# Performance work log

Hardware: AMD Instinct MI355X
Metric: run time of the kernel (lower is better)

Reference implementation:

```python
import jax, jax.numpy as jnp
import numpy as np

HEADS = 4
DIM_HEAD = 32
EPS = 1e-5


def setup_inputs() -> dict:
    key = jax.random.key(0)
    ks = jax.random.split(key, 4)
    B, dim, H, W = 8, 256, 128, 128
    hidden = HEADS * DIM_HEAD  # 128
    x = jax.random.normal(ks[0], (B, dim, H, W), dtype=jnp.float32)
    # 1x1 conv weights stored as [out_ch, in_ch]
    qkv_w = jax.random.normal(ks[1], (3 * hidden, dim), dtype=jnp.float32) * (1.0 / np.sqrt(dim))
    conv_w = jax.random.normal(ks[2], (dim, hidden), dtype=jnp.float32) * (1.0 / np.sqrt(hidden))
    conv_b = jax.random.normal(ks[3], (dim,), dtype=jnp.float32) * 0.01
    gamma = jnp.ones((dim,), dtype=jnp.float32)
    beta = jnp.zeros((dim,), dtype=jnp.float32)
    return {"x": x, "qkv_w": qkv_w, "conv_w": conv_w, "conv_b": conv_b,
            "gamma": gamma, "beta": beta}


def reference(x, qkv_w, conv_w, conv_b, gamma, beta):
    B, C, H, W = x.shape
    N = H * W
    scale = DIM_HEAD ** (-0.5)
    # qkv 1x1 conv -> [B, 3, heads, dim_head, N]
    qkv = jnp.einsum('oc,bchw->bohw', qkv_w, x).reshape(B, 3, HEADS, DIM_HEAD, N)
    q, k, v = qkv[:, 0], qkv[:, 1], qkv[:, 2]
    q = jax.nn.softmax(q, axis=-2) * scale   # softmax over dim_head axis
    k = jax.nn.softmax(k, axis=-1)           # softmax over spatial axis
    v = v / N
    # context = k @ v^T : [B, h, d, d]
    context = jnp.einsum('bhdn,bhen->bhde', k, v)
    # out = context @ q : [B, h, d, N]
    out = jnp.einsum('bhde,bhen->bhdn', context, q)
    out = out.reshape(B, HEADS * DIM_HEAD, H, W)
    # final 1x1 conv with bias
    y = jnp.einsum('oc,bchw->bohw', conv_w, out) + conv_b[None, :, None, None]
    # InstanceNorm2d(affine=True): per-sample per-channel over (H, W), biased var
    mean = jnp.mean(y, axis=(2, 3), keepdims=True)
    var = jnp.var(y, axis=(2, 3), keepdims=True)
    y = (y - mean) * jax.lax.rsqrt(var + EPS)
    return y * gamma[None, :, None, None] + beta[None, :, None, None]
```

## Files before the change

### kernel.cpp

```cpp
#include <hip/hip_runtime.h>
#include <math.h>

#define NPIX 16384
#define DIMC 256
#define BATCH 8
#define HEADS 4
#define DHEAD 32
#define HID 128
#define OQKV 384
#define EPS 1e-5f
#define SCALE 0.17677669529663687f

typedef _Float16 f16x8 __attribute__((ext_vector_type(8)));
typedef float f32x4 __attribute__((ext_vector_type(4)));

__device__ inline void gl_lds16(const void* g, void* l) {
    __builtin_amdgcn_global_load_lds(
        (const __attribute__((address_space(1))) unsigned*)g,
        (__attribute__((address_space(3))) unsigned*)l, 16, 0, 0);
}

__global__ __launch_bounds__(256) void prep_kernel(
    const float* __restrict__ qkv_w, const float* __restrict__ conv_w,
    _Float16* __restrict__ wh, _Float16* __restrict__ ch, float* __restrict__ zbuf)
{
    int i = blockIdx.x * 256 + threadIdx.x;
    if (i < 98304) wh[i] = (_Float16)qkv_w[i];
    else           ch[i - 98304] = (_Float16)conv_w[i - 98304];
    if (i < 33792) zbuf[i] = 0.f;
}

__global__ __launch_bounds__(256) void transpose_x(const float* __restrict__ x,
                                                   _Float16* __restrict__ xh)
{
    __shared__ float tile[64][65];
    int t = threadIdx.x;
    int n0 = blockIdx.x * 64;
    int c0 = blockIdx.y * 64;
    int b  = blockIdx.z;
    const float* xb = x + (long)b * DIMC * NPIX;
    #pragma unroll
    for (int it = 0; it < 4; it++) {
        int c  = it * 16 + (t >> 4);
        int n4 = (t & 15) * 4;
        float4 v = *(const float4*)&xb[(long)(c0 + c) * NPIX + n0 + n4];
        tile[c][n4] = v.x; tile[c][n4+1] = v.y; tile[c][n4+2] = v.z; tile[c][n4+3] = v.w;
    }
    __syncthreads();
    _Float16* xo = xh + (long)b * NPIX * DIMC;
    #pragma unroll
    for (int it = 0; it < 2; it++) {
        int n  = it * 32 + (t >> 3);
        int c8 = (t & 7) * 8;
        f16x8 o;
        #pragma unroll
        for (int k = 0; k < 8; k++) o[k] = (_Float16)tile[c8 + k][n];
        *(f16x8*)&xo[(long)(n0 + n) * DIMC + c0 + c8] = o;
    }
}

template<int K>
__global__ __launch_bounds__(256) void gemm_h(
    const _Float16* __restrict__ A,
    const _Float16* __restrict__ Bm,
    _Float16* __restrict__ Cm,
    long bsB, long bsC)
{
    __shared__ _Float16 As[128 * 32];
    __shared__ _Float16 Bs[128 * 32];
    const int t = threadIdx.x;
    const int n0 = blockIdx.x * 128;
    const int m0 = blockIdx.y * 128;
    const _Float16* Bb = Bm + (long)blockIdx.z * bsB;
    const int w = t >> 6, lane = t & 63;
    const int q = lane >> 4, l16 = lane & 15;
    const int mw = (w >> 1) * 64, nw = (w & 1) * 64;

    f32x4 acc[4][4] = {};

    for (int k0 = 0; k0 < K; k0 += 32) {
        #pragma unroll
        for (int is = 0; is < 2; is++) {
            int idx = is * 256 + t;
            int row = idx >> 2, kc = (idx & 3) * 8;
            gl_lds16(&A [(long)(m0 + row) * K + k0 + kc], &As[idx * 8]);
            gl_lds16(&Bb[(long)(n0 + row) * K + k0 + kc], &Bs[idx * 8]);
        }
        __syncthreads();
        f16x8 af[4], bf[4];
        #pragma unroll
        for (int i = 0; i < 4; i++) {
            af[i] = *(const f16x8*)&As[(mw + i * 16 + l16) * 32 + q * 8];
            bf[i] = *(const f16x8*)&Bs[(nw + i * 16 + l16) * 32 + q * 8];
        }
        #pragma unroll
        for (int i = 0; i < 4; i++)
            #pragma unroll
            for (int j = 0; j < 4; j++)
                acc[i][j] = __builtin_amdgcn_mfma_f32_16x16x32_f16(af[i], bf[j], acc[i][j], 0, 0, 0);
        __syncthreads();
    }

    _Float16* Cb = Cm + (long)blockIdx.z * bsC;
    #pragma unroll
    for (int i = 0; i < 4; i++) {
        int rbase = m0 + mw + i * 16 + q * 4;
        #pragma unroll
        for (int j = 0; j < 4; j++) {
            int col = n0 + nw + j * 16 + l16;
            #pragma unroll
            for (int r = 0; r < 4; r++)
                Cb[(long)(rbase + r) * NPIX + col] = (_Float16)acc[i][j][r];
        }
    }
}

__global__ __launch_bounds__(256) void kmax_h(const _Float16* __restrict__ qkvh,
                                              float* __restrict__ kmax)
{
    int rr = blockIdx.x;
    int b = rr >> 7, oo = rr & 127;
    const _Float16* row = qkvh + ((long)b * OQKV + HID + oo) * NPIX;
    int t = threadIdx.x;
    float m = -1e30f;
    #pragma unroll
    for (int i = 0; i < 8; i++) {
        f16x8 v = *(const f16x8*)&row[(i * 256 + t) * 8];
        #pragma unroll
        for (int k = 0; k < 8; k++) m = fmaxf(m, (float)v[k]);
    }
    for (int off = 32; off > 0; off >>= 1) m = fmaxf(m, __shfl_down(m, off));
    __shared__ float sm[4];
    if ((t & 63) == 0) sm[t >> 6] = m;
    __syncthreads();
    if (t == 0) kmax[rr] = fmaxf(fmaxf(sm[0], sm[1]), fmaxf(sm[2], sm[3]));
}

__global__ __launch_bounds__(256) void ctx_h(const _Float16* __restrict__ qkvh,
    const float* __restrict__ kmax, float* __restrict__ ctx_raw, float* __restrict__ ksum)
{
    __shared__ float ek[32][129];
    __shared__ float vv[32][129];
    __shared__ float cbuf[4][1024];
    int tid = threadIdx.x;
    int chunk = blockIdx.x, bh = blockIdx.y;
    int b = bh >> 2, h = bh & 3;
    const _Float16* kbase = qkvh + ((long)b * OQKV + HID + h * DHEAD) * NPIX;
    const _Float16* vbase = qkvh + ((long)b * OQKV + 2 * HID + h * DHEAD) * NPIX;
    int r = tid >> 3, c8 = tid & 7;
    float m = kmax[bh * DHEAD + r];
    float spart = 0.f;
    int g = tid >> 6, tg = tid & 63;
    int d0 = (tg >> 3) * 4, e0 = (tg & 7) * 4;
    float acc[4][4] = {{0}};

    for (int sub = 0; sub < 8; sub++) {
        int n0 = chunk * 1024 + sub * 128;
        #pragma unroll
        for (int jj = 0; jj < 2; jj++) {
            int col = c8 * 16 + jj * 8;
            f16x8 kv = *(const f16x8*)&kbase[(long)r * NPIX + n0 + col];
            f16x8 vf = *(const f16x8*)&vbase[(long)r * NPIX + n0 + col];
            #pragma unroll
            for (int ii = 0; ii < 8; ii++) {
                float e = __expf((float)kv[ii] - m);
                ek[r][col + ii] = e; spart += e;
                vv[r][col + ii] = (float)vf[ii];
            }
        }
        __syncthreads();
        #pragma unroll 4
        for (int i = 0; i < 32; i++) {
            int n = g * 32 + i;
            float ekv[4], vvv[4];
            #pragma unroll
            for (int d = 0; d < 4; d++) ekv[d] = ek[d0 + d][n];
            #pragma unroll
            for (int e = 0; e < 4; e++) vvv[e] = vv[e0 + e][n];
            #pragma unroll
            for (int d = 0; d < 4; d++)
                #pragma unroll
                for (int e = 0; e < 4; e++) acc[d][e] += ekv[d] * vvv[e];
        }
        __syncthreads();
    }
    for (int off = 4; off > 0; off >>= 1) spart += __shfl_down(spart, off, 8);
    if (c8 == 0) atomicAdd(&ksum[bh * DHEAD + r], spart);
    #pragma unroll
    for (int d = 0; d < 4; d++)
        #pragma unroll
        for (int e = 0; e < 4; e++) cbuf[g][(d0 + d) * 32 + (e0 + e)] = acc[d][e];
    __syncthreads();
    #pragma unroll
    for (int ii = 0; ii < 4; ii++) {
        int idx = ii * 256 + tid;
        float s = cbuf[0][idx] + cbuf[1][idx] + cbuf[2][idx] + cbuf[3][idx];
        atomicAdd(&ctx_raw[(long)bh * 1024 + idx], s);
    }
}

__global__ __launch_bounds__(256) void outq_h(_Float16* __restrict__ qkvh,
    const float* __restrict__ ctx_raw, const float* __restrict__ ksum)
{
    __shared__ float ctx_t[4][32][32];
    int tid = threadIdx.x;
    int n = blockIdx.x * 256 + tid;
    int b = blockIdx.y;
    #pragma unroll
    for (int i = 0; i < 16; i++) {
        int idx = i * 256 + tid;
        int h = idx >> 10, de = idx & 1023;
        int d = de >> 5, e = de & 31;
        float s = ksum[(b * 4 + h) * DHEAD + d];
        ctx_t[h][e][d] = SCALE * ctx_raw[(long)(b * 4 + h) * 1024 + de] / s;
    }
    __syncthreads();
    _Float16* ob = qkvh + ((long)b * OQKV + 2 * HID) * NPIX + (long)n * HID;
    for (int h = 0; h < 4; h++) {
        const _Float16* qb = qkvh + ((long)b * OQKV + h * DHEAD) * NPIX + n;
        float qv[32];
        float mx = -1e30f;
        #pragma unroll
        for (int e = 0; e < 32; e++) { qv[e] = (float)qb[(long)e * NPIX]; mx = fmaxf(mx, qv[e]); }
        float s = 0.f;
        #pragma unroll
        for (int e = 0; e < 32; e++) { qv[e] = __expf(qv[e] - mx); s += qv[e]; }
        float qs = 1.f / s;
        float4 o4[8];
        #pragma unroll
        for (int j = 0; j < 8; j++) o4[j] = make_float4(0,0,0,0);
        #pragma unroll 8
        for (int e = 0; e < 32; e++) {
            float qe = qv[e] * qs;
            #pragma unroll
            for (int j = 0; j < 8; j++) {
                float4 c = *(const float4*)&ctx_t[h][e][j * 4];
                o4[j].x += c.x * qe; o4[j].y += c.y * qe;
                o4[j].z += c.z * qe; o4[j].w += c.w * qe;
            }
        }
        #pragma unroll
        for (int j = 0; j < 4; j++) {
            f16x8 pk;
            float4 a = o4[j * 2], bb = o4[j * 2 + 1];
            pk[0] = (_Float16)a.x;  pk[1] = (_Float16)a.y;
            pk[2] = (_Float16)a.z;  pk[3] = (_Float16)a.w;
            pk[4] = (_Float16)bb.x; pk[5] = (_Float16)bb.y;
            pk[6] = (_Float16)bb.z; pk[7] = (_Float16)bb.w;
            *(f16x8*)&ob[h * DHEAD + j * 8] = pk;
        }
    }
}

__global__ __launch_bounds__(256) void ln_stats(const _Float16* __restrict__ yh,
    const float* __restrict__ gamma, const float* __restrict__ beta,
    float* __restrict__ mv)
{
    int row = blockIdx.x;
    int t = threadIdx.x;
    const _Float16* p = yh + (long)row * NPIX;
    float s = 0.f, sq = 0.f;
    #pragma unroll
    for (int i = 0; i < 8; i++) {
        f16x8 v = *(const f16x8*)&p[(i * 256 + t) * 8];
        #pragma unroll
        for (int k = 0; k < 8; k++) { float f = (float)v[k]; s += f; sq += f * f; }
    }
    for (int off = 32; off > 0; off >>= 1) { s += __shfl_down(s, off); sq += __shfl_down(sq, off); }
    __shared__ float ss[4], ssq[4];
    if ((t & 63) == 0) { ss[t >> 6] = s; ssq[t >> 6] = sq; }
    __syncthreads();
    if (t == 0) {
        s  = ss[0] + ss[1] + ss[2] + ss[3];
        sq = ssq[0] + ssq[1] + ssq[2] + ssq[3];
        float meanp = s * (1.f / NPIX);
        float varp  = fmaxf(sq * (1.f / NPIX) - meanp * meanp, 0.f);
        float rinv  = rsqrtf(varp * (1.f / ((float)NPIX * (float)NPIX)) + EPS);
        int c = row & 255;
        float g = rinv * gamma[c];
        mv[row * 2]     = g * (1.f / NPIX);
        mv[row * 2 + 1] = beta[c] - meanp * (1.f / NPIX) * g;
    }
}

__global__ __launch_bounds__(256) void ln_apply(const _Float16* __restrict__ yh,
    const float* __restrict__ mv, float* __restrict__ out)
{
    long i8 = (long)blockIdx.x * 256 + threadIdx.x;
    int row = (int)(i8 >> 11);
    float a = mv[row * 2], be = mv[row * 2 + 1];
    f16x8 v = *(const f16x8*)&yh[i8 * 8];
    float4 o1, o2;
    o1.x = (float)v[0] * a + be; o1.y = (float)v[1] * a + be;
    o1.z = (float)v[2] * a + be; o1.w = (float)v[3] * a + be;
    o2.x = (float)v[4] * a + be; o2.y = (float)v[5] * a + be;
    o2.z = (float)v[6] * a + be; o2.w = (float)v[7] * a + be;
    *(float4*)&out[i8 * 8]     = o1;
    *(float4*)&out[i8 * 8 + 4] = o2;
}

extern "C" void kernel_launch(void* const* d_in, const int* in_sizes, int n_in,
                              void* d_out, int out_size, void* d_ws, size_t ws_size,
                              hipStream_t stream)
{
    const float* x      = (const float*)d_in[0];
    const float* qkv_w  = (const float*)d_in[1];
    const float* conv_w = (const float*)d_in[2];
    const float* gamma  = (const float*)d_in[4];
    const float* beta   = (const float*)d_in[5];
    float* out = (float*)d_out;

    _Float16* xh   = (_Float16*)d_ws;
    _Float16* qkvh = xh + 33554432;
    _Float16* wh   = qkvh + 50331648;
    _Float16* ch   = wh + 98304;
    float* stats   = (float*)(ch + 32768);
    float* ctx_raw = stats;
    float* ksum    = ctx_raw + 32768;
    float* kmaxp   = ksum + 1024;
    float* mv      = kmaxp + 1024;
    _Float16* yh   = xh;

    prep_kernel<<<512, 256, 0, stream>>>(qkv_w, conv_w, wh, ch, ctx_raw);
    transpose_x<<<dim3(256, 4, BATCH), 256, 0, stream>>>(x, xh);
    gemm_h<256><<<dim3(128, 3, BATCH), 256, 0, stream>>>(
        wh, xh, qkvh, (long)NPIX * DIMC, (long)OQKV * NPIX);
    kmax_h<<<1024, 256, 0, stream>>>(qkvh, kmaxp);
    ctx_h<<<dim3(16, 32), 256, 0, stream>>>(qkvh, kmaxp, ctx_raw, ksum);
    outq_h<<<dim3(64, BATCH), 256, 0, stream>>>(qkvh, ctx_raw, ksum);
    gemm_h<128><<<dim3(128, 2, BATCH), 256, 0, stream>>>(
        ch, qkvh + (long)2 * HID * NPIX, yh, (long)OQKV * NPIX, (long)DIMC * NPIX);
    ln_stats<<<2048, 256, 0, stream>>>(yh, gamma, beta, mv);
    ln_apply<<<16384, 256, 0, stream>>>(yh, mv, out);
}
```

Before: 414.4 us.

## Fuse instance-norm stats into GEMM epilogue, MFMA context, drop kmax pass

The GEMM epilogue now stages C through swizzled LDS so global stores are 16-byte vectors, and the second GEMM also accumulates per-row sum and sum-of-squares via atomics. That replaces the separate ln_stats pass over the output. The context kernel is rewritten to use MFMA with f16 exp(k) computed in registers, and the kmax reduction kernel is removed (exp without max subtraction). The grid order is swapped so batch is the fastest-varying dimension. Dropping the max subtraction risks overflow for large k values, and many atomics are added in the epilogue.

```diff
diff --git a/kernel.cpp b/kernel.cpp
--- a/kernel.cpp
+++ b/kernel.cpp
@@ -27,7 +27,7 @@
     int i = blockIdx.x * 256 + threadIdx.x;
     if (i < 98304) wh[i] = (_Float16)qkv_w[i];
     else           ch[i - 98304] = (_Float16)conv_w[i - 98304];
-    if (i < 33792) zbuf[i] = 0.f;
+    if (i < 37888) zbuf[i] = 0.f;
 }
 
 __global__ __launch_bounds__(256) void transpose_x(const float* __restrict__ x,
@@ -59,19 +59,21 @@
     }
 }
 
-template<int K>
+template<int K, int EPI>
 __global__ __launch_bounds__(256) void gemm_h(
     const _Float16* __restrict__ A,
     const _Float16* __restrict__ Bm,
     _Float16* __restrict__ Cm,
-    long bsB, long bsC)
-{
-    __shared__ _Float16 As[128 * 32];
-    __shared__ _Float16 Bs[128 * 32];
-    const int t = threadIdx.x;
-    const int n0 = blockIdx.x * 128;
+    long bsB, long bsC, float* __restrict__ lnacc)
+{
+    __shared__ _Float16 smem[16384];
+    _Float16* As = smem;
+    _Float16* Bs = smem + 4096;
+    const int t  = threadIdx.x;
+    const int b  = blockIdx.x;
     const int m0 = blockIdx.y * 128;
-    const _Float16* Bb = Bm + (long)blockIdx.z * bsB;
+    const int n0 = blockIdx.z * 128;
+    const _Float16* Bb = Bm + (long)b * bsB;
     const int w = t >> 6, lane = t & 63;
     const int q = lane >> 4, l16 = lane & 15;
     const int mw = (w >> 1) * 64, nw = (w & 1) * 64;
@@ -101,99 +103,97 @@
         __syncthreads();
     }
 
-    _Float16* Cb = Cm + (long)blockIdx.z * bsC;
+    _Float16* Cs = smem;
     #pragma unroll
     for (int i = 0; i < 4; i++) {
-        int rbase = m0 + mw + i * 16 + q * 4;
         #pragma unroll
         for (int j = 0; j < 4; j++) {
-            int col = n0 + nw + j * 16 + l16;
-            #pragma unroll
-            for (int r = 0; r < 4; r++)
-                Cb[(long)(rbase + r) * NPIX + col] = (_Float16)acc[i][j][r];
-        }
-    }
-}
-
-__global__ __launch_bounds__(256) void kmax_h(const _Float16* __restrict__ qkvh,
-                                              float* __restrict__ kmax)
-{
-    int rr = blockIdx.x;
-    int b = rr >> 7, oo = rr & 127;
-    const _Float16* row = qkvh + ((long)b * OQKV + HID + oo) * NPIX;
+            #pragma unroll
+            for (int r = 0; r < 4; r++) {
+                int row = mw + i * 16 + q * 4 + r;
+                int col = nw + j * 16 + l16;
+                Cs[row * 128 + (col ^ ((row & 15) << 3))] = (_Float16)acc[i][j][r];
+            }
+        }
+    }
+    __syncthreads();
+    _Float16* Cb = Cm + (long)b * bsC;
+    #pragma unroll
+    for (int it = 0; it < 8; it++) {
+        int u = it * 256 + t;
+        int row = u >> 4, cg = u & 15;
+        f16x8 v8 = *(const f16x8*)&Cs[row * 128 + ((cg * 8) ^ ((row & 15) << 3))];
+        *(f16x8*)&Cb[(long)(m0 + row) * NPIX + n0 + cg * 8] = v8;
+        if (EPI) {
+            float s = 0.f, sq = 0.f;
+            #pragma unroll
+            for (int k = 0; k < 8; k++) { float f = (float)v8[k]; s += f; sq += f * f; }
+            #pragma unroll
+            for (int off = 8; off > 0; off >>= 1) {
+                s  += __shfl_down(s,  off, 16);
+                sq += __shfl_down(sq, off, 16);
+            }
+            if ((t & 15) == 0) {
+                int rg = b * DIMC + m0 + row;
+                atomicAdd(&lnacc[rg * 2],     s);
+                atomicAdd(&lnacc[rg * 2 + 1], sq);
+            }
+        }
+    }
+}
+
+__global__ __launch_bounds__(256) void ctx_mfma(const _Float16* __restrict__ qkvh,
+    float* __restrict__ ctx_raw, float* __restrict__ ksum)
+{
+    __shared__ float cbuf[4][1024];
     int t = threadIdx.x;
-    float m = -1e30f;
-    #pragma unroll
-    for (int i = 0; i < 8; i++) {
-        f16x8 v = *(const f16x8*)&row[(i * 256 + t) * 8];
-        #pragma unroll
-        for (int k = 0; k < 8; k++) m = fmaxf(m, (float)v[k]);
-    }
-    for (int off = 32; off > 0; off >>= 1) m = fmaxf(m, __shfl_down(m, off));
-    __shared__ float sm[4];
-    if ((t & 63) == 0) sm[t >> 6] = m;
+    int w = t >> 6, lane = t & 63;
+    int q = lane >> 4, l16 = lane & 15;
+    int bh = blockIdx.y, b = bh >> 2, h = bh & 3;
+    const _Float16* kb = qkvh + ((long)b * OQKV + HID + h * DHEAD) * NPIX;
+    const _Float16* vb = qkvh + ((long)b * OQKV + 2 * HID + h * DHEAD) * NPIX;
+    long n0 = (long)blockIdx.x * 2048 + w * 512 + q * 8;
+
+    f32x4 c00 = {}, c01 = {}, c10 = {}, c11 = {};
+    float ks0 = 0.f, ks1 = 0.f;
+
+    for (int s = 0; s < 16; s++) {
+        long n = n0 + s * 32;
+        f16x8 kf0 = *(const f16x8*)&kb[(long)l16 * NPIX + n];
+        f16x8 kf1 = *(const f16x8*)&kb[(long)(16 + l16) * NPIX + n];
+        f16x8 vf0 = *(const f16x8*)&vb[(long)l16 * NPIX + n];
+        f16x8 vf1 = *(const f16x8*)&vb[(long)(16 + l16) * NPIX + n];
+        f16x8 e0, e1;
+        #pragma unroll
+        for (int j = 0; j < 8; j++) {
+            float ea = __expf((float)kf0[j]); e0[j] = (_Float16)ea; ks0 += ea;
+            float eb = __expf((float)kf1[j]); e1[j] = (_Float16)eb; ks1 += eb;
+        }
+        c00 = __builtin_amdgcn_mfma_f32_16x16x32_f16(e0, vf0, c00, 0, 0, 0);
+        c01 = __builtin_amdgcn_mfma_f32_16x16x32_f16(e0, vf1, c01, 0, 0, 0);
+        c10 = __builtin_amdgcn_mfma_f32_16x16x32_f16(e1, vf0, c10, 0, 0, 0);
+        c11 = __builtin_amdgcn_mfma_f32_16x16x32_f16(e1, vf1, c11, 0, 0, 0);
+    }
+
+    ks0 += __shfl_down(ks0, 32); ks0 += __shfl_down(ks0, 16);
+    ks1 += __shfl_down(ks1, 32); ks1 += __shfl_down(ks1, 16);
+    if (lane < 16) {
+        atomicAdd(&ksum[bh * DHEAD + l16],      ks0);
+        atomicAdd(&ksum[bh * DHEAD + 16 + l16], ks1);
+    }
+
+    float* cb = cbuf[w];
+    #pragma unroll
+    for (int r = 0; r < 4; r++) {
+        cb[(q * 4 + r) * 32 + l16]            = c00[r];
+        cb[(q * 4 + r) * 32 + 16 + l16]       = c01[r];
+        cb[(16 + q * 4 + r) * 32 + l16]       = c10[r];
+        cb[(16 + q * 4 + r) * 32 + 16 + l16]  = c11[r];
+    }
     __syncthreads();
-    if (t == 0) kmax[rr] = fmaxf(fmaxf(sm[0], sm[1]), fmaxf(sm[2], sm[3]));
-}
-
-__global__ __launch_bounds__(256) void ctx_h(const _Float16* __restrict__ qkvh,
-    const float* __restrict__ kmax, float* __restrict__ ctx_raw, float* __restrict__ ksum)
-{
-    __shared__ float ek[32][129];
-    __shared__ float vv[32][129];
-    __shared__ float cbuf[4][1024];
-    int tid = threadIdx.x;
-    int chunk = blockIdx.x, bh = blockIdx.y;
-    int b = bh >> 2, h = bh & 3;
-    const _Float16* kbase = qkvh + ((long)b * OQKV + HID + h * DHEAD) * NPIX;
-    const _Float16* vbase = qkvh + ((long)b * OQKV + 2 * HID + h * DHEAD) * NPIX;
-    int r = tid >> 3, c8 = tid & 7;
-    float m = kmax[bh * DHEAD + r];
-    float spart = 0.f;
-    int g = tid >> 6, tg = tid & 63;
-    int d0 = (tg >> 3) * 4, e0 = (tg & 7) * 4;
-    float acc[4][4] = {{0}};
-
-    for (int sub = 0; sub < 8; sub++) {
-        int n0 = chunk * 1024 + sub * 128;
-        #pragma unroll
-        for (int jj = 0; jj < 2; jj++) {
-            int col = c8 * 16 + jj * 8;
-            f16x8 kv = *(const f16x8*)&kbase[(long)r * NPIX + n0 + col];
-            f16x8 vf = *(const f16x8*)&vbase[(long)r * NPIX + n0 + col];
-            #pragma unroll
-            for (int ii = 0; ii < 8; ii++) {
-                float e = __expf((float)kv[ii] - m);
-                ek[r][col + ii] = e; spart += e;
-                vv[r][col + ii] = (float)vf[ii];
-            }
-        }
-        __syncthreads();
-        #pragma unroll 4
-        for (int i = 0; i < 32; i++) {
-            int n = g * 32 + i;
-            float ekv[4], vvv[4];
-            #pragma unroll
-            for (int d = 0; d < 4; d++) ekv[d] = ek[d0 + d][n];
-            #pragma unroll
-            for (int e = 0; e < 4; e++) vvv[e] = vv[e0 + e][n];
-            #pragma unroll
-            for (int d = 0; d < 4; d++)
-                #pragma unroll
-                for (int e = 0; e < 4; e++) acc[d][e] += ekv[d] * vvv[e];
-        }
-        __syncthreads();
-    }
-    for (int off = 4; off > 0; off >>= 1) spart += __shfl_down(spart, off, 8);
-    if (c8 == 0) atomicAdd(&ksum[bh * DHEAD + r], spart);
-    #pragma unroll
-    for (int d = 0; d < 4; d++)
-        #pragma unroll
-        for (int e = 0; e < 4; e++) cbuf[g][(d0 + d) * 32 + (e0 + e)] = acc[d][e];
-    __syncthreads();
     #pragma unroll
     for (int ii = 0; ii < 4; ii++) {
-        int idx = ii * 256 + tid;
+        int idx = ii * 256 + t;
         float s = cbuf[0][idx] + cbuf[1][idx] + cbuf[2][idx] + cbuf[3][idx];
         atomicAdd(&ctx_raw[(long)bh * 1024 + idx], s);
     }
@@ -252,35 +252,19 @@
     }
 }
 
-__global__ __launch_bounds__(256) void ln_stats(const _Float16* __restrict__ yh,
+__global__ __launch_bounds__(256) void ln_finalize(const float* __restrict__ lnacc,
     const float* __restrict__ gamma, const float* __restrict__ beta,
     float* __restrict__ mv)
 {
-    int row = blockIdx.x;
-    int t = threadIdx.x;
-    const _Float16* p = yh + (long)row * NPIX;
-    float s = 0.f, sq = 0.f;
-    #pragma unroll
-    for (int i = 0; i < 8; i++) {
-        f16x8 v = *(const f16x8*)&p[(i * 256 + t) * 8];
-        #pragma unroll
-        for (int k = 0; k < 8; k++) { float f = (float)v[k]; s += f; sq += f * f; }
-    }
-    for (int off = 32; off > 0; off >>= 1) { s += __shfl_down(s, off); sq += __shfl_down(sq, off); }
-    __shared__ float ss[4], ssq[4];
-    if ((t & 63) == 0) { ss[t >> 6] = s; ssq[t >> 6] = sq; }
-    __syncthreads();
-    if (t == 0) {
-        s  = ss[0] + ss[1] + ss[2] + ss[3];
-        sq = ssq[0] + ssq[1] + ssq[2] + ssq[3];
-        float meanp = s * (1.f / NPIX);
-        float varp  = fmaxf(sq * (1.f / NPIX) - meanp * meanp, 0.f);
-        float rinv  = rsqrtf(varp * (1.f / ((float)NPIX * (float)NPIX)) + EPS);
-        int c = row & 255;
-        float g = rinv * gamma[c];
-        mv[row * 2]     = g * (1.f / NPIX);
-        mv[row * 2 + 1] = beta[c] - meanp * (1.f / NPIX) * g;
-    }
+    int row = blockIdx.x * 256 + threadIdx.x;
+    float s = lnacc[row * 2], sq = lnacc[row * 2 + 1];
+    float meanp = s * (1.f / NPIX);
+    float varp  = fmaxf(sq * (1.f / NPIX) - meanp * meanp, 0.f);
+    float rinv  = rsqrtf(varp * (1.f / ((float)NPIX * (float)NPIX)) + EPS);
+    int c = row & 255;
+    float g = rinv * gamma[c];
+    mv[row * 2]     = g * (1.f / NPIX);
+    mv[row * 2 + 1] = beta[c] - meanp * (1.f / NPIX) * g;
 }
 
 __global__ __launch_bounds__(256) void ln_apply(const _Float16* __restrict__ yh,
@@ -314,22 +298,20 @@
     _Float16* qkvh = xh + 33554432;
     _Float16* wh   = qkvh + 50331648;
     _Float16* ch   = wh + 98304;
-    float* stats   = (float*)(ch + 32768);
-    float* ctx_raw = stats;
+    float* ctx_raw = (float*)(ch + 32768);
     float* ksum    = ctx_raw + 32768;
-    float* kmaxp   = ksum + 1024;
-    float* mv      = kmaxp + 1024;
+    float* lnacc   = ksum + 1024;
+    float* mv      = lnacc + 4096;
     _Float16* yh   = xh;
 
     prep_kernel<<<512, 256, 0, stream>>>(qkv_w, conv_w, wh, ch, ctx_raw);
     transpose_x<<<dim3(256, 4, BATCH), 256, 0, stream>>>(x, xh);
-    gemm_h<256><<<dim3(128, 3, BATCH), 256, 0, stream>>>(
-        wh, xh, qkvh, (long)NPIX * DIMC, (long)OQKV * NPIX);
-    kmax_h<<<1024, 256, 0, stream>>>(qkvh, kmaxp);
-    ctx_h<<<dim3(16, 32), 256, 0, stream>>>(qkvh, kmaxp, ctx_raw, ksum);
+    gemm_h<256, 0><<<dim3(BATCH, 3, 128), 256, 0, stream>>>(
+        wh, xh, qkvh, (long)NPIX * DIMC, (long)OQKV * NPIX, nullptr);
+    ctx_mfma<<<dim3(8, 32), 256, 0, stream>>>(qkvh, ctx_raw, ksum);
     outq_h<<<dim3(64, BATCH), 256, 0, stream>>>(qkvh, ctx_raw, ksum);
-    gemm_h<128><<<dim3(128, 2, BATCH), 256, 0, stream>>>(
-        ch, qkvh + (long)2 * HID * NPIX, yh, (long)OQKV * NPIX, (long)DIMC * NPIX);
-    ln_stats<<<2048, 256, 0, stream>>>(yh, gamma, beta, mv);
+    gemm_h<128, 1><<<dim3(BATCH, 2, 128), 256, 0, stream>>>(
+        ch, qkvh + (long)2 * HID * NPIX, yh, (long)OQKV * NPIX, (long)DIMC * NPIX, lnacc);
+    ln_finalize<<<8, 256, 0, stream>>>(lnacc, gamma, beta, mv);
     ln_apply<<<16384, 256, 0, stream>>>(yh, mv, out);
 }
```

After: 396.2 us. 4.4% less time.
